# Performance work log

Hardware: AMD Instinct MI355X
Metric: run time of the kernel (lower is better)

## Reference

```python
import jax, jax.numpy as jnp
import numpy as np

K = 2  # DGL TAGConv default number of hops
N_GRAPHS = 64


def _tag_conv(h, src, dst, W, b, norm):
    # TAGConv: concat [h, A_hat h, A_hat^2 h] @ W + b, A_hat = D^-1/2 A D^-1/2
    n = h.shape[0]
    hops = [h]
    cur = h
    for _ in range(K):
        msg = (cur * norm)[src]                      # gather from src, [E, d]
        agg = jnp.zeros_like(cur).at[dst].add(msg)   # scatter-sum to dst
        cur = agg * norm
        hops.append(cur)
    z = jnp.concatenate(hops, axis=-1)               # [N, (K+1)*d]
    return jax.nn.relu(z @ W + b)


def _norm(dst, n):
    deg = jnp.zeros((n,), jnp.float32).at[dst].add(1.0)
    deg = jnp.clip(deg, 1.0, None)
    return (deg ** -0.5)[:, None]                    # [N, 1]


def setup_inputs() -> dict:
    key = jax.random.key(0)
    ks = jax.random.split(key, 8)
    N, E, IN, HID, C = 100000, 3200000, 128, 256, 10
    h = jax.random.normal(ks[0], (N, IN), jnp.float32)
    src = jax.random.randint(ks[1], (E,), 0, N, jnp.int32)
    dst = jax.random.randint(ks[2], (E,), 0, N, jnp.int32)
    graph_ids = jnp.sort(jax.random.randint(ks[3], (N,), 0, N_GRAPHS, jnp.int32))
    s1 = ((K + 1) * IN) ** -0.5
    s2 = ((K + 1) * HID) ** -0.5
    W1 = jax.random.normal(ks[4], ((K + 1) * IN, HID), jnp.float32) * s1
    b1 = jnp.zeros((HID,), jnp.float32)
    W2 = jax.random.normal(ks[5], ((K + 1) * HID, HID), jnp.float32) * s2
    b2 = jnp.zeros((HID,), jnp.float32)
    Wc = jax.random.normal(ks[6], (HID, C), jnp.float32) * (HID ** -0.5)
    bc = jnp.zeros((C,), jnp.float32)
    return {"h": h, "src": src, "dst": dst, "graph_ids": graph_ids,
            "W1": W1, "b1": b1, "W2": W2, "b2": b2, "Wc": Wc, "bc": bc}


def reference(h, src, dst, graph_ids, W1, b1, W2, b2, Wc, bc):
    n = h.shape[0]
    norm = _norm(dst, n)
    x = _tag_conv(h, src, dst, W1, b1, norm)
    x = _tag_conv(x, src, dst, W2, b2, norm)
    pooled = jax.ops.segment_max(x, graph_ids, num_segments=N_GRAPHS)  # [G, HID]
    return pooled @ Wc + bc                                            # [G, C]
```

## Files before the change

kernel.cpp:

```cpp
#include <hip/hip_runtime.h>
#include <hip/hip_bf16.h>


typedef unsigned short u16;
typedef unsigned int u32;
typedef unsigned char u8;

__device__ inline float u2f(u16 u) { return __uint_as_float(((u32)u) << 16); }
__device__ inline u16 f2u(float f) {
    __hip_bfloat16 b = __float2bfloat16(f);
    return *reinterpret_cast<u16*>(&b);
}


constexpr int NPB = 128, NC = 128, NBMAX = 784;

__global__ __launch_bounds__(256) void countA_kernel(
    const int* __restrict__ dst, int* __restrict__ Hmat, int E, int CS, int NB) {
    __shared__ int hist[NBMAX];
    int tid = threadIdx.x;
    for (int b = tid; b < NB; b += 256) hist[b] = 0;
    __syncthreads();
    int base = blockIdx.x * CS;
    int end = base + CS < E ? base + CS : E;
    for (int i = base + tid; i < end; i += 256) {
        int d = __builtin_nontemporal_load(dst + i);
        atomicAdd(&hist[d >> 7], 1);
    }
    __syncthreads();
    for (int b = tid; b < NB; b += 256) Hmat[b * NC + blockIdx.x] = hist[b];
}

__global__ __launch_bounds__(256) void scatterC_kernel(
    const int* __restrict__ src, const int* __restrict__ dst,
    const int* __restrict__ Omat, uint2* __restrict__ Earr,
    int E, int CS, int NB) {
    __shared__ int cur[NBMAX];
    int tid = threadIdx.x;
    int c = blockIdx.x;
    for (int b = tid; b < NB; b += 256) cur[b] = Omat[b * NC + c];
    __syncthreads();
    int base = c * CS;
    int end = base + CS < E ? base + CS : E;
    for (int i = base + tid; i < end; i += 256) {
        int d = __builtin_nontemporal_load(dst + i);
        int s = __builtin_nontemporal_load(src + i);
        int pos = atomicAdd(&cur[d >> 7], 1);
        uint2 e;
        e.x = (u32)s;
        e.y = (u32)(d & (NPB - 1));
        Earr[pos] = e;
    }
}

__global__ __launch_bounds__(256) void fineD_kernel(
    const uint2* __restrict__ Earr, const int* __restrict__ Omat,
    int* __restrict__ colidx, int* __restrict__ rowptr,
    float* __restrict__ normv, int N, int E, int NB) {
    __shared__ int cnt[NPB];
    __shared__ int scn[NPB];
    __shared__ int cur2[NPB];
    int tid = threadIdx.x;
    int b = blockIdx.x;
    int base = Omat[b * NC];
    int end = Omat[(b + 1) * NC];
    if (tid < NPB) cnt[tid] = 0;
    __syncthreads();
    for (int i = base + tid; i < end; i += 256)
        atomicAdd(&cnt[Earr[i].y], 1);
    __syncthreads();
    if (tid < NPB) scn[tid] = cnt[tid];
    __syncthreads();
    for (int off = 1; off < NPB; off <<= 1) {
        int v = (tid < NPB && tid >= off) ? scn[tid - off] : 0;
        __syncthreads();
        if (tid < NPB) scn[tid] += v;
        __syncthreads();
    }
    int node0 = b * NPB;
    if (tid < NPB) {
        int excl = scn[tid] - cnt[tid];
        cur2[tid] = base + excl;
        int node = node0 + tid;
        if (node < N) {
            rowptr[node] = base + excl;
            int d = cnt[tid];
            float fd = d < 1 ? 1.0f : (float)d;
            normv[node] = rsqrtf(fd);
        }
    }
    if (b == 0 && tid == 0) rowptr[N] = E;
    __syncthreads();
    for (int i = base + tid; i < end; i += 256) {
        uint2 e = Earr[i];
        int pos = atomicAdd(&cur2[e.y], 1);
        colidx[pos] = (int)e.x;
    }
}

__global__ void scan1_kernel(const int* __restrict__ in, int* __restrict__ outp,
                             int* __restrict__ bsum, int n) {
    __shared__ int sd[1024];
    int t = threadIdx.x;
    int i = blockIdx.x * 1024 + t;
    int v = (i < n) ? in[i] : 0;
    sd[t] = v;
    __syncthreads();
    for (int off = 1; off < 1024; off <<= 1) {
        int x = (t >= off) ? sd[t - off] : 0;
        __syncthreads();
        sd[t] += x;
        __syncthreads();
    }
    if (i < n) outp[i] = sd[t] - v;
    if (t == 1023) bsum[blockIdx.x] = sd[t];
}

__global__ void scan2_kernel(int* __restrict__ bsum, int nb) {
    __shared__ int sd[1024];
    int t = threadIdx.x;
    int v = (t < nb) ? bsum[t] : 0;
    sd[t] = v;
    __syncthreads();
    for (int off = 1; off < 1024; off <<= 1) {
        int x = (t >= off) ? sd[t - off] : 0;
        __syncthreads();
        sd[t] += x;
        __syncthreads();
    }
    if (t < nb) bsum[t] = sd[t] - v;
}

__global__ void scan3_kernel(int* __restrict__ outp, const int* __restrict__ bsum,
                             int n, int E) {
    int i = blockIdx.x * blockDim.x + threadIdx.x;
    if (i < n) outp[i] += bsum[i >> 10];
    if (i == 0) outp[n] = E;
}


struct alignas(4) U2 { u16 v[2]; };
struct alignas(8) U4 { u16 v[4]; };
struct alignas(16) U8 { u16 v[8]; };


__global__ __launch_bounds__(256) void castquant_f32_128(
    const float* __restrict__ h, u16* __restrict__ cat, int ldcat,
    const float* __restrict__ normv,
    u8* __restrict__ q, float* __restrict__ m, int N) {
    int row = blockIdx.x * 4 + (threadIdx.x >> 6);
    if (row >= N) return;
    int lane = threadIdx.x & 63;
    float2 f = *(const float2*)(h + (size_t)row * 128 + lane * 2);
    U2 o;
    o.v[0] = f2u(f.x);
    o.v[1] = f2u(f.y);
    *(U2*)(cat + (size_t)row * ldcat + lane * 2) = o;
    float mx = fmaxf(fabsf(f.x), fabsf(f.y));
    #pragma unroll
    for (int off = 32; off > 0; off >>= 1)
        mx = fmaxf(mx, __shfl_xor(mx, off, 64));
    float inv = mx > 0.f ? 127.f / mx : 0.f;
    u32 q0 = (u32)((int)rintf(f.x * inv) + 128);
    u32 q1 = (u32)((int)rintf(f.y * inv) + 128);
    *(unsigned short*)(q + (size_t)row * 128 + lane * 2) =
        (unsigned short)(q0 | (q1 << 8));
    if (lane == 0) m[row] = normv[row] * (mx * (1.f / 127.f));
}


__global__ __launch_bounds__(256) void quant_bf16_256(
    const u16* __restrict__ x, const float* __restrict__ normv,
    u8* __restrict__ q, float* __restrict__ m, int N) {
    int row = blockIdx.x * 4 + (threadIdx.x >> 6);
    if (row >= N) return;
    int lane = threadIdx.x & 63;
    U4 v = *(const U4*)(x + (size_t)row * 256 + lane * 4);
    float f[4];
    #pragma unroll
    for (int i = 0; i < 4; ++i) f[i] = u2f(v.v[i]);
    float mx = fmaxf(fmaxf(fabsf(f[0]), fabsf(f[1])),
                     fmaxf(fabsf(f[2]), fabsf(f[3])));
    #pragma unroll
    for (int off = 32; off > 0; off >>= 1)
        mx = fmaxf(mx, __shfl_xor(mx, off, 64));
    float inv = mx > 0.f ? 127.f / mx : 0.f;
    u32 b0 = (u32)((int)rintf(f[0] * inv) + 128);
    u32 b1 = (u32)((int)rintf(f[1] * inv) + 128);
    u32 b2 = (u32)((int)rintf(f[2] * inv) + 128);
    u32 b3 = (u32)((int)rintf(f[3] * inv) + 128);
    *(u32*)(q + (size_t)row * 256 + lane * 4) =
        b0 | (b1 << 8) | (b2 << 16) | (b3 << 24);
    if (lane == 0) m[row] = normv[row] * (mx * (1.f / 127.f));
}


template <int BPL, int QOUT>
__global__ __launch_bounds__(256, 2) void prop_q8_kernel(
    const u8* __restrict__ qin, const float* __restrict__ m,
    u16* __restrict__ out, int ldout,
    const int* __restrict__ rowptr, const int* __restrict__ colidx,
    const float* __restrict__ normv, int N,
    u8* __restrict__ qout, float* __restrict__ mout) {
    constexpr int D = 32 * BPL;
    constexpr int NW = BPL / 4;
    constexpr int UE = 8;
    int node = blockIdx.x * 4 + (threadIdx.x >> 6);
    if (node >= N) return;
    const int lane = threadIdx.x & 63;
    const int half = lane >> 5;
    const int l32 = lane & 31;
    const u32 laneoff = (u32)l32 * BPL;
    int s = rowptr[node], e = rowptr[node + 1];
    float acc[BPL];
    #pragma unroll
    for (int q = 0; q < BPL; ++q) acc[q] = 0.f;
    float msum = 0.f;
    const int nfull = (e - s) >> 4;
    int p = s;
    if (nfull > 0) {
        int c[UE];
        #pragma unroll
        for (int u = 0; u < UE; ++u) c[u] = colidx[s + 2 * u + half];
        for (int g = 0; g < nfull; ++g) {
            u32 w[UE][NW];
            #pragma unroll
            for (int u = 0; u < UE; ++u) {
                u32 off = (u32)c[u] * D + laneoff;
                if (BPL == 8) {
                    uint2 gg = *(const uint2*)(qin + off);
                    w[u][0] = gg.x; w[u][1] = gg.y;
                } else {
                    w[u][0] = *(const u32*)(qin + off);
                }
            }
            float nm[UE];
            #pragma unroll
            for (int u = 0; u < UE; ++u) nm[u] = m[c[u]];
            if (g + 1 < nfull) {
                int pn = s + (g + 1) * 16;
                #pragma unroll
                for (int u = 0; u < UE; ++u) c[u] = colidx[pn + 2 * u + half];
            }
            #pragma unroll
            for (int u = 0; u < UE; ++u) {
                msum += nm[u];
                #pragma unroll
                for (int t = 0; t < NW; ++t) {
                    u32 ww = w[u][t];
                    acc[4 * t + 0] += nm[u] * (float)(ww & 0xffu);
                    acc[4 * t + 1] += nm[u] * (float)((ww >> 8) & 0xffu);
                    acc[4 * t + 2] += nm[u] * (float)((ww >> 16) & 0xffu);
                    acc[4 * t + 3] += nm[u] * (float)(ww >> 24);
                }
            }
        }
        p = s + nfull * 16;
    }
    if (p < e) {
        const int el = e - 1;
        int c[UE];
        #pragma unroll
        for (int u = 0; u < UE; ++u) {
            int idx = p + 2 * u + half;
            c[u] = colidx[idx < e ? idx : el];
        }
        u32 w[UE][NW];
        #pragma unroll
        for (int u = 0; u < UE; ++u) {
            u32 off = (u32)c[u] * D + laneoff;
            if (BPL == 8) {
                uint2 gg = *(const uint2*)(qin + off);
                w[u][0] = gg.x; w[u][1] = gg.y;
            } else {
                w[u][0] = *(const u32*)(qin + off);
            }
        }
        float nm[UE];
        #pragma unroll
        for (int u = 0; u < UE; ++u) {
            int idx = p + 2 * u + half;
            float mm = m[c[u]];
            nm[u] = idx < e ? mm : 0.f;
        }
        #pragma unroll
        for (int u = 0; u < UE; ++u) {
            msum += nm[u];
            #pragma unroll
            for (int t = 0; t < NW; ++t) {
                u32 ww = w[u][t];
                acc[4 * t + 0] += nm[u] * (float)(ww & 0xffu);
                acc[4 * t + 1] += nm[u] * (float)((ww >> 8) & 0xffu);
                acc[4 * t + 2] += nm[u] * (float)((ww >> 16) & 0xffu);
                acc[4 * t + 3] += nm[u] * (float)(ww >> 24);
            }
        }
    }
    #pragma unroll
    for (int q = 0; q < BPL; ++q) acc[q] += __shfl_xor(acc[q], 32, 64);
    msum += __shfl_xor(msum, 32, 64);
    float nn = normv[node];
    #pragma unroll
    for (int q = 0; q < BPL; ++q) acc[q] = nn * (acc[q] - 128.f * msum);
    if (half == 0) {
        if (BPL == 8) {
            U8 o;
            #pragma unroll
            for (int q = 0; q < 8; ++q) o.v[q] = f2u(acc[q]);
            *(U8*)(out + (size_t)node * ldout + l32 * 8) = o;
        } else {
            U4 o;
            #pragma unroll
            for (int q = 0; q < 4; ++q) o.v[q] = f2u(acc[q]);
            *(U4*)(out + (size_t)node * ldout + l32 * 4) = o;
        }
    }
    if (QOUT) {
        float mx = 0.f;
        #pragma unroll
        for (int q = 0; q < BPL; ++q) mx = fmaxf(mx, fabsf(acc[q]));
        #pragma unroll
        for (int off = 16; off > 0; off >>= 1)
            mx = fmaxf(mx, __shfl_xor(mx, off, 64));
        float inv = mx > 0.f ? 127.f / mx : 0.f;
        if (half == 0) {
            u32 b[BPL > 4 ? 8 : 4];
            #pragma unroll
            for (int q = 0; q < BPL; ++q)
                b[q] = (u32)((int)rintf(acc[q] * inv) + 128);
            if (BPL == 8) {
                uint2 g;
                g.x = b[0] | (b[1] << 8) | (b[2] << 16) | (b[3] << 24);
                g.y = b[4] | (b[5] << 8) | (b[6] << 16) | (b[7] << 24);
                *(uint2*)(qout + (size_t)node * D + l32 * 8) = g;
            } else {
                *(u32*)(qout + (size_t)node * D + l32 * 4) =
                    b[0] | (b[1] << 8) | (b[2] << 16) | (b[3] << 24);
            }
            if (lane == 0) mout[node] = nn * (mx * (1.f / 127.f));
        }
    }
}


typedef __attribute__((ext_vector_type(8))) short bf16x8f;
typedef __attribute__((ext_vector_type(4))) float f32x4;

__device__ inline void async16(const void* g, void* l) {
    __builtin_amdgcn_global_load_lds(
        (__attribute__((address_space(1))) void*)(g),
        (__attribute__((address_space(3))) void*)(l), 16, 0, 0);
}

constexpr int GBM = 128, GBN = 128, GBK = 32;

__device__ inline void stage_panel(const u16* __restrict__ P, int ldp, int row0,
                                   int k0, u16* dst, int tid) {
    #pragma unroll
    for (int i = 0; i < 2; ++i) {
        int c = tid + i * 256;
        int row = c >> 2;
        int seg = (c & 3) ^ ((row >> 1) & 3);
        async16(P + (size_t)(row0 + row) * ldp + k0 + seg * 8, dst + c * 8);
    }
}

template <int KK>
__global__ __launch_bounds__(256) void gemm_mfma(
    const u16* __restrict__ A, int lda,
    const u16* __restrict__ Bt,
    const u16* __restrict__ Cadd,
    const float* __restrict__ bias,
    u16* __restrict__ Cout,
    int M, int relu) {
    __shared__ u16 Ab[2][GBM * GBK];
    __shared__ u16 Bb[2][GBN * GBK];
    const int tid = threadIdx.x;
    const int lane = tid & 63;
    const int wave = tid >> 6;
    const int wm = wave >> 1, wn = wave & 1;
    int nwg = gridDim.x;
    int qq = nwg >> 3, rr = nwg & 7;
    int xcd = blockIdx.x & 7, wi = blockIdx.x >> 3;
    int nb = (xcd < rr ? xcd * (qq + 1) : rr * (qq + 1) + (xcd - rr) * qq) + wi;
    const int row0 = (nb >> 1) * GBM;
    const int col0 = (nb & 1) * GBN;
    const int NOUT = 256;

    stage_panel(A, lda, row0, 0, Ab[0], tid);
    stage_panel(Bt, KK, col0, 0, Bb[0], tid);
    __syncthreads();

    f32x4 acc[4][4];
    #pragma unroll
    for (int mi = 0; mi < 4; ++mi)
        #pragma unroll
        for (int ni = 0; ni < 4; ++ni) acc[mi][ni] = (f32x4)0.f;

    constexpr int nk = KK / GBK;
    const int mb = lane & 15;
    const int seg = lane >> 4;
    for (int ks = 0; ks < nk; ++ks) {
        int cur = ks & 1;
        if (ks + 1 < nk) {
            stage_panel(A, lda, row0, (ks + 1) * GBK, Ab[cur ^ 1], tid);
            stage_panel(Bt, KK, col0, (ks + 1) * GBK, Bb[cur ^ 1], tid);
        }
        bf16x8f a[4], b[4];
        #pragma unroll
        for (int mi = 0; mi < 4; ++mi) {
            int r = wm * 64 + mi * 16 + mb;
            int ca = r * 4 + (seg ^ ((r >> 1) & 3));
            a[mi] = *(const bf16x8f*)&Ab[cur][ca * 8];
        }
        #pragma unroll
        for (int ni = 0; ni < 4; ++ni) {
            int n = wn * 64 + ni * 16 + mb;
            int cb = n * 4 + (seg ^ ((n >> 1) & 3));
            b[ni] = *(const bf16x8f*)&Bb[cur][cb * 8];
        }
        #pragma unroll
        for (int mi = 0; mi < 4; ++mi)
            #pragma unroll
            for (int ni = 0; ni < 4; ++ni)
                acc[mi][ni] = __builtin_amdgcn_mfma_f32_16x16x32_bf16(
                    a[mi], b[ni], acc[mi][ni], 0, 0, 0);
        __syncthreads();
    }

    #pragma unroll
    for (int mi = 0; mi < 4; ++mi) {
        #pragma unroll
        for (int r = 0; r < 4; ++r) {
            int row = row0 + wm * 64 + mi * 16 + (lane >> 4) * 4 + r;
            if (row < M) {
                #pragma unroll
                for (int ni = 0; ni < 4; ++ni) {
                    int col = col0 + wn * 64 + ni * 16 + (lane & 15);
                    float v = acc[mi][ni][r];
                    if (Cadd) v += u2f(Cadd[(size_t)row * NOUT + col]);
                    if (bias) v += bias[col];
                    if (relu) v = fmaxf(v, 0.f);
                    Cout[(size_t)row * NOUT + col] = f2u(v);
                }
            }
        }
    }
}

__global__ void transpose_cast(const float* __restrict__ W, u16* __restrict__ Wt,
                               int K, int Nn) {
    int idx = blockIdx.x * blockDim.x + threadIdx.x;
    if (idx < K * Nn) {
        int n = idx / K, k = idx % K;
        Wt[idx] = f2u(W[(size_t)k * Nn + n]);
    }
}


__global__ void pool_kernel(const u16* __restrict__ x, const int* __restrict__ gid,
                            float* __restrict__ pooled, int N, int HID) {
    int t = threadIdx.x;
    int n0 = blockIdx.x * 128;
    int n1 = n0 + 128 < N ? n0 + 128 : N;
    float cur = 0.f;
    int cg = gid[n0];
    for (int n = n0; n < n1; ++n) {
        int g = gid[n];
        if (g != cg) {
            atomicMax((int*)&pooled[(size_t)cg * HID + t], __float_as_int(cur));
            cg = g;
            cur = 0.f;
        }
        float v = u2f(x[(size_t)n * HID + t]);
        cur = cur > v ? cur : v;
    }
    atomicMax((int*)&pooled[(size_t)cg * HID + t], __float_as_int(cur));
}

__global__ void head_kernel(const float* __restrict__ pooled, const float* __restrict__ Wc,
                            const float* __restrict__ bc, float* __restrict__ out,
                            int HID, int C) {
    __shared__ float row[256];
    int g = blockIdx.x;
    int t = threadIdx.x;
    if (t < HID) row[t] = pooled[(size_t)g * HID + t];
    __syncthreads();
    if (t < C) {
        float s = bc[t];
        for (int k = 0; k < HID; ++k) s += row[k] * Wc[(size_t)k * C + t];
        out[(size_t)g * C + t] = s;
    }
}


extern "C" void kernel_launch(void* const* d_in, const int* in_sizes, int n_in,
                              void* d_out, int out_size, void* d_ws, size_t ws_size,
                              hipStream_t stream) {
    const float* h  = (const float*)d_in[0];
    const int* src  = (const int*)d_in[1];
    const int* dst  = (const int*)d_in[2];
    const int* gid  = (const int*)d_in[3];
    const float* W1 = (const float*)d_in[4];
    const float* b1 = (const float*)d_in[5];
    const float* W2 = (const float*)d_in[6];
    const float* b2 = (const float*)d_in[7];
    const float* Wc = (const float*)d_in[8];
    const float* bc = (const float*)d_in[9];
    float* out = (float*)d_out;

    const int N   = in_sizes[3];
    const int E   = in_sizes[1];
    const int IN  = in_sizes[0] / N;
    const int HID = in_sizes[5];
    const int C   = in_sizes[9];
    const int G   = out_size / C;
    const int CAT = 3 * IN;
    const int Mpad = (N + 127) & ~127;
    const int NB = (N + NPB - 1) / NPB;
    const int CS = (E + NC - 1) / NC;

    char* wp = (char*)d_ws;
    auto alloc = [&](size_t bytes) {
        char* p = wp;
        wp += (bytes + 255) & ~(size_t)255;
        return p;
    };
    float* pooled = (float*)alloc((size_t)G * HID * sizeof(float));
    float* normv  = (float*)alloc((size_t)N * sizeof(float));
    float* mv     = (float*)alloc((size_t)N * sizeof(float));
    float* mv2    = (float*)alloc((size_t)N * sizeof(float));
    int* rowptr   = (int*)alloc((size_t)(N + 1) * sizeof(int));
    int* bsum     = (int*)alloc(1024 * sizeof(int));
    int* Omat     = (int*)alloc((size_t)(NB * NC + 1) * sizeof(int));
    int* Hmat     = (int*)alloc((size_t)(NB * NC) * sizeof(int));
    int* colidx   = (int*)alloc((size_t)E * sizeof(int));
    u16* Wt1      = (u16*)alloc((size_t)CAT * HID * sizeof(u16));
    u16* Wt2      = (u16*)alloc((size_t)3 * HID * HID * sizeof(u16));
    u16* CAT1     = (u16*)alloc((size_t)Mpad * CAT * sizeof(u16));
    u16* X1       = (u16*)alloc((size_t)Mpad * HID * sizeof(u16));
    u16* B2       = (u16*)alloc((size_t)Mpad * HID * sizeof(u16));
    u16* B1       = CAT1;
    uint2* Earr   = (uint2*)CAT1;
    u8* Q8L2      = (u8*)(CAT1 + (size_t)Mpad * HID);
    u8* Q8A       = (u8*)B2;
    u8* Q8B       = (u8*)B2 + (size_t)Mpad * 128;

    const int n2 = NB * NC;
    countA_kernel<<<NC, 256, 0, stream>>>(dst, Hmat, E, CS, NB);
    scan1_kernel<<<(n2 + 1023) / 1024, 1024, 0, stream>>>(Hmat, Omat, bsum, n2);
    scan2_kernel<<<1, 1024, 0, stream>>>(bsum, (n2 + 1023) / 1024);
    scan3_kernel<<<(n2 + 255) / 256, 256, 0, stream>>>(Omat, bsum, n2, E);
    scatterC_kernel<<<NC, 256, 0, stream>>>(src, dst, Omat, Earr, E, CS, NB);
    fineD_kernel<<<NB, 256, 0, stream>>>(Earr, Omat, colidx, rowptr, normv, N, E, NB);

    transpose_cast<<<(CAT * HID + 255) / 256, 256, 0, stream>>>(W1, Wt1, CAT, HID);
    for (int s2 = 0; s2 < 3; ++s2)
        transpose_cast<<<(HID * HID + 255) / 256, 256, 0, stream>>>(
            W2 + (size_t)s2 * HID * HID, Wt2 + (size_t)s2 * HID * HID, HID, HID);

    int pb = (N + 3) / 4;
    castquant_f32_128<<<pb, 256, 0, stream>>>(h, CAT1, CAT, normv, Q8A, mv, N);
    prop_q8_kernel<4, 1><<<pb, 256, 0, stream>>>(Q8A, mv, CAT1 + IN, CAT,
                                                 rowptr, colidx, normv, N, Q8B, mv2);
    prop_q8_kernel<4, 0><<<pb, 256, 0, stream>>>(Q8B, mv2, CAT1 + 2 * IN, CAT,
                                                 rowptr, colidx, normv, N,
                                                 nullptr, nullptr);
    int nwg = (Mpad / GBM) * (HID / GBN);
    gemm_mfma<384><<<nwg, 256, 0, stream>>>(CAT1, CAT, Wt1, nullptr, b1, X1, N, 1);

    gemm_mfma<256><<<nwg, 256, 0, stream>>>(X1, HID, Wt2 + (size_t)2 * HID * HID,
                                            nullptr, nullptr, B1, N, 0);
    quant_bf16_256<<<pb, 256, 0, stream>>>(B1, normv, Q8L2, mv, N);
    prop_q8_kernel<8, 0><<<pb, 256, 0, stream>>>(Q8L2, mv, B2, HID,
                                                 rowptr, colidx, normv, N,
                                                 nullptr, nullptr);
    gemm_mfma<256><<<nwg, 256, 0, stream>>>(X1, HID, Wt2 + (size_t)HID * HID,
                                            B2, nullptr, B1, N, 0);
    quant_bf16_256<<<pb, 256, 0, stream>>>(B1, normv, Q8L2, mv, N);
    prop_q8_kernel<8, 0><<<pb, 256, 0, stream>>>(Q8L2, mv, B2, HID,
                                                 rowptr, colidx, normv, N,
                                                 nullptr, nullptr);
    gemm_mfma<256><<<nwg, 256, 0, stream>>>(X1, HID, Wt2, B2, b2, B1, N, 1);

    hipMemsetAsync(pooled, 0, (size_t)G * HID * sizeof(float), stream);
    pool_kernel<<<(N + 127) / 128, HID, 0, stream>>>(B1, gid, pooled, N, HID);
    head_kernel<<<G, HID, 0, stream>>>(pooled, Wc, bc, out, HID, C);
}
```

Baseline: 1.050 ms.

## Stage GEMM K in 128-wide phases instead of double-buffered 32-wide slices

Replaces the double-buffered 32-wide K pipeline with single-buffered 128-wide K phases. Each phase loads the whole panel into LDS with a new XOR swizzle, then runs four MFMA k-steps, which cuts the number of barriers per tile. It also adds a launch_bounds occupancy hint of two blocks per CU. The cost is losing load/compute overlap inside a block, and the 64 KB of LDS per block limits residency.

```diff
diff --git a/kernel.cpp b/kernel.cpp
--- a/kernel.cpp
+++ b/kernel.cpp
@@ -352,29 +352,19 @@
         (__attribute__((address_space(3))) void*)(l), 16, 0, 0);
 }
 
-constexpr int GBM = 128, GBN = 128, GBK = 32;
-
-__device__ inline void stage_panel(const u16* __restrict__ P, int ldp, int row0,
-                                   int k0, u16* dst, int tid) {
-    #pragma unroll
-    for (int i = 0; i < 2; ++i) {
-        int c = tid + i * 256;
-        int row = c >> 2;
-        int seg = (c & 3) ^ ((row >> 1) & 3);
-        async16(P + (size_t)(row0 + row) * ldp + k0 + seg * 8, dst + c * 8);
-    }
-}
+constexpr int GBM = 128, GBN = 128, GBK = 32, KH = 128;
 
 template <int KK>
-__global__ __launch_bounds__(256) void gemm_mfma(
+__global__ __launch_bounds__(256, 2) void gemm_mfma(
     const u16* __restrict__ A, int lda,
     const u16* __restrict__ Bt,
     const u16* __restrict__ Cadd,
     const float* __restrict__ bias,
     u16* __restrict__ Cout,
     int M, int relu) {
-    __shared__ u16 Ab[2][GBM * GBK];
-    __shared__ u16 Bb[2][GBN * GBK];
+    constexpr int NPH = KK / KH;
+    __shared__ u16 Ab[GBM * KH];
+    __shared__ u16 Bb[GBN * KH];
     const int tid = threadIdx.x;
     const int lane = tid & 63;
     const int wave = tid >> 6;
@@ -387,45 +377,57 @@
     const int col0 = (nb & 1) * GBN;
     const int NOUT = 256;
 
-    stage_panel(A, lda, row0, 0, Ab[0], tid);
-    stage_panel(Bt, KK, col0, 0, Bb[0], tid);
-    __syncthreads();
-
     f32x4 acc[4][4];
     #pragma unroll
     for (int mi = 0; mi < 4; ++mi)
         #pragma unroll
         for (int ni = 0; ni < 4; ++ni) acc[mi][ni] = (f32x4)0.f;
 
-    constexpr int nk = KK / GBK;
     const int mb = lane & 15;
-    const int seg = lane >> 4;
-    for (int ks = 0; ks < nk; ++ks) {
-        int cur = ks & 1;
-        if (ks + 1 < nk) {
-            stage_panel(A, lda, row0, (ks + 1) * GBK, Ab[cur ^ 1], tid);
-            stage_panel(Bt, KK, col0, (ks + 1) * GBK, Bb[cur ^ 1], tid);
-        }
-        bf16x8f a[4], b[4];
-        #pragma unroll
-        for (int mi = 0; mi < 4; ++mi) {
-            int r = wm * 64 + mi * 16 + mb;
-            int ca = r * 4 + (seg ^ ((r >> 1) & 3));
-            a[mi] = *(const bf16x8f*)&Ab[cur][ca * 8];
-        }
-        #pragma unroll
-        for (int ni = 0; ni < 4; ++ni) {
-            int n = wn * 64 + ni * 16 + mb;
-            int cb = n * 4 + (seg ^ ((n >> 1) & 3));
-            b[ni] = *(const bf16x8f*)&Bb[cur][cb * 8];
-        }
-        #pragma unroll
-        for (int mi = 0; mi < 4; ++mi)
-            #pragma unroll
-            for (int ni = 0; ni < 4; ++ni)
-                acc[mi][ni] = __builtin_amdgcn_mfma_f32_16x16x32_bf16(
-                    a[mi], b[ni], acc[mi][ni], 0, 0, 0);
-        __syncthreads();
+    const int seg4 = lane >> 4;
+
+    for (int ph = 0; ph < NPH; ++ph) {
+        if (ph) __syncthreads();
+        #pragma unroll
+        for (int i = 0; i < 8; ++i) {
+            int c = tid + i * 256;
+            int row = c >> 4;
+            int sg = (c & 15) ^ (row & 7);
+            async16(A + (size_t)(row0 + row) * lda + ph * KH + sg * 8,
+                    Ab + c * 8);
+        }
+        #pragma unroll
+        for (int i = 0; i < 8; ++i) {
+            int c = tid + i * 256;
+            int row = c >> 4;
+            int sg = (c & 15) ^ (row & 7);
+            async16(Bt + (size_t)(col0 + row) * KK + ph * KH + sg * 8,
+                    Bb + c * 8);
+        }
+        __syncthreads();
+        #pragma unroll
+        for (int ks = 0; ks < KH / GBK; ++ks) {
+            int j = ks * 4 + seg4;
+            bf16x8f a[4], b[4];
+            #pragma unroll
+            for (int mi = 0; mi < 4; ++mi) {
+                int r = wm * 64 + mi * 16 + mb;
+                int ca = r * 16 + (j ^ (r & 7));
+                a[mi] = *(const bf16x8f*)&Ab[ca * 8];
+            }
+            #pragma unroll
+            for (int ni = 0; ni < 4; ++ni) {
+                int n = wn * 64 + ni * 16 + mb;
+                int cb = n * 16 + (j ^ (n & 7));
+                b[ni] = *(const bf16x8f*)&Bb[cb * 8];
+            }
+            #pragma unroll
+            for (int mi = 0; mi < 4; ++mi)
+                #pragma unroll
+                for (int ni = 0; ni < 4; ++ni)
+                    acc[mi][ni] = __builtin_amdgcn_mfma_f32_16x16x32_bf16(
+                        a[mi], b[ni], acc[mi][ni], 0, 0, 0);
+        }
     }
 
     #pragma unroll
```

Measured after the change: 1.012 ms. 1.04x faster.

## Replace LDS-staged GEMM with per-wave register-direct MFMA tiles

Applied to the files above, without the earlier changes.

Swaps the shared-memory double-buffered 128x128 block GEMM for a kernel where each wave independently computes a 128x32 output tile. Each wave loads A and B fragments straight from global memory into registers and feeds them to MFMA, with no LDS staging and no block-level syncs. This removes LDS traffic and barrier overhead and allows more resident blocks per CU. In exchange, the reuse of A across columns now depends on L2/L1 caching instead of shared memory, so each A row panel is fetched by eight separate waves.

```diff
diff --git a/kernel.cpp b/kernel.cpp
--- a/kernel.cpp
+++ b/kernel.cpp
@@ -346,100 +346,73 @@
 typedef __attribute__((ext_vector_type(8))) short bf16x8f;
 typedef __attribute__((ext_vector_type(4))) float f32x4;
 
-__device__ inline void async16(const void* g, void* l) {
-    __builtin_amdgcn_global_load_lds(
-        (__attribute__((address_space(1))) void*)(g),
-        (__attribute__((address_space(3))) void*)(l), 16, 0, 0);
-}
-
-constexpr int GBM = 128, GBN = 128, GBK = 32;
-
-__device__ inline void stage_panel(const u16* __restrict__ P, int ldp, int row0,
-                                   int k0, u16* dst, int tid) {
-    #pragma unroll
-    for (int i = 0; i < 2; ++i) {
-        int c = tid + i * 256;
-        int row = c >> 2;
-        int seg = (c & 3) ^ ((row >> 1) & 3);
-        async16(P + (size_t)(row0 + row) * ldp + k0 + seg * 8, dst + c * 8);
-    }
-}
-
 template <int KK>
-__global__ __launch_bounds__(256) void gemm_mfma(
-    const u16* __restrict__ A, int lda,
+__global__ __launch_bounds__(256, 3) void gemm_wave(
+    const u16* __restrict__ A,
     const u16* __restrict__ Bt,
     const u16* __restrict__ Cadd,
     const float* __restrict__ bias,
     u16* __restrict__ Cout,
-    int M, int relu) {
-    __shared__ u16 Ab[2][GBM * GBK];
-    __shared__ u16 Bb[2][GBN * GBK];
+    int M, int NJOBS, int relu) {
     const int tid = threadIdx.x;
     const int lane = tid & 63;
     const int wave = tid >> 6;
-    const int wm = wave >> 1, wn = wave & 1;
     int nwg = gridDim.x;
     int qq = nwg >> 3, rr = nwg & 7;
     int xcd = blockIdx.x & 7, wi = blockIdx.x >> 3;
-    int nb = (xcd < rr ? xcd * (qq + 1) : rr * (qq + 1) + (xcd - rr) * qq) + wi;
-    const int row0 = (nb >> 1) * GBM;
-    const int col0 = (nb & 1) * GBN;
-    const int NOUT = 256;
-
-    stage_panel(A, lda, row0, 0, Ab[0], tid);
-    stage_panel(Bt, KK, col0, 0, Bb[0], tid);
-    __syncthreads();
-
-    f32x4 acc[4][4];
-    #pragma unroll
-    for (int mi = 0; mi < 4; ++mi)
-        #pragma unroll
-        for (int ni = 0; ni < 4; ++ni) acc[mi][ni] = (f32x4)0.f;
-
-    constexpr int nk = KK / GBK;
+    int slot = (xcd < rr ? xcd * (qq + 1) : rr * (qq + 1) + (xcd - rr) * qq) + wi;
+    int job = slot * 4 + wave;
+    if (job >= NJOBS) return;
+    const int rt = job >> 3;
+    const int cg = job & 7;
+    const int row0 = rt << 7;
+    const int col0 = cg << 5;
     const int mb = lane & 15;
     const int seg = lane >> 4;
-    for (int ks = 0; ks < nk; ++ks) {
-        int cur = ks & 1;
-        if (ks + 1 < nk) {
-            stage_panel(A, lda, row0, (ks + 1) * GBK, Ab[cur ^ 1], tid);
-            stage_panel(Bt, KK, col0, (ks + 1) * GBK, Bb[cur ^ 1], tid);
-        }
-        bf16x8f a[4], b[4];
-        #pragma unroll
-        for (int mi = 0; mi < 4; ++mi) {
-            int r = wm * 64 + mi * 16 + mb;
-            int ca = r * 4 + (seg ^ ((r >> 1) & 3));
-            a[mi] = *(const bf16x8f*)&Ab[cur][ca * 8];
-        }
-        #pragma unroll
-        for (int ni = 0; ni < 4; ++ni) {
-            int n = wn * 64 + ni * 16 + mb;
-            int cb = n * 4 + (seg ^ ((n >> 1) & 3));
-            b[ni] = *(const bf16x8f*)&Bb[cur][cb * 8];
-        }
-        #pragma unroll
-        for (int mi = 0; mi < 4; ++mi)
-            #pragma unroll
-            for (int ni = 0; ni < 4; ++ni)
-                acc[mi][ni] = __builtin_amdgcn_mfma_f32_16x16x32_bf16(
-                    a[mi], b[ni], acc[mi][ni], 0, 0, 0);
-        __syncthreads();
-    }
-
-    #pragma unroll
-    for (int mi = 0; mi < 4; ++mi) {
+    const int NOUT = 256;
+
+    const u16* pA = A + (size_t)(row0 + mb) * KK + seg * 8;
+    const u16* pB = Bt + (size_t)(col0 + mb) * KK + seg * 8;
+
+    f32x4 acc[8][2];
+    #pragma unroll
+    for (int mi = 0; mi < 8; ++mi) {
+        acc[mi][0] = (f32x4)0.f;
+        acc[mi][1] = (f32x4)0.f;
+    }
+
+    #pragma unroll
+    for (int j = 0; j < KK / 32; ++j) {
+        bf16x8f b0 = *(const bf16x8f*)(pB + (size_t)0 * 16 * KK + j * 32);
+        bf16x8f b1 = *(const bf16x8f*)(pB + (size_t)16 * KK + j * 32);
+        bf16x8f a[8];
+        #pragma unroll
+        for (int mi = 0; mi < 8; ++mi)
+            a[mi] = *(const bf16x8f*)(pA + (size_t)mi * 16 * KK + j * 32);
+        #pragma unroll
+        for (int mi = 0; mi < 8; ++mi) {
+            acc[mi][0] = __builtin_amdgcn_mfma_f32_16x16x32_bf16(
+                a[mi], b0, acc[mi][0], 0, 0, 0);
+            acc[mi][1] = __builtin_amdgcn_mfma_f32_16x16x32_bf16(
+                a[mi], b1, acc[mi][1], 0, 0, 0);
+        }
+    }
+
+    float bv[2];
+    bv[0] = bias ? bias[col0 + 0 * 16 + mb] : 0.f;
+    bv[1] = bias ? bias[col0 + 1 * 16 + mb] : 0.f;
+    #pragma unroll
+    for (int mi = 0; mi < 8; ++mi) {
         #pragma unroll
         for (int r = 0; r < 4; ++r) {
-            int row = row0 + wm * 64 + mi * 16 + (lane >> 4) * 4 + r;
+            int row = row0 + mi * 16 + seg * 4 + r;
             if (row < M) {
                 #pragma unroll
-                for (int ni = 0; ni < 4; ++ni) {
-                    int col = col0 + wn * 64 + ni * 16 + (lane & 15);
+                for (int ni = 0; ni < 2; ++ni) {
+                    int col = col0 + ni * 16 + mb;
                     float v = acc[mi][ni][r];
                     if (Cadd) v += u2f(Cadd[(size_t)row * NOUT + col]);
-                    if (bias) v += bias[col];
+                    v += bv[ni];
                     if (relu) v = fmaxf(v, 0.f);
                     Cout[(size_t)row * NOUT + col] = f2u(v);
                 }
@@ -566,22 +539,23 @@
     prop_q8_kernel<4, 0><<<pb, 256, 0, stream>>>(Q8B, mv2, CAT1 + 2 * IN, CAT,
                                                  rowptr, colidx, normv, N,
                                                  nullptr, nullptr);
-    int nwg = (Mpad / GBM) * (HID / GBN);
-    gemm_mfma<384><<<nwg, 256, 0, stream>>>(CAT1, CAT, Wt1, nullptr, b1, X1, N, 1);
-
-    gemm_mfma<256><<<nwg, 256, 0, stream>>>(X1, HID, Wt2 + (size_t)2 * HID * HID,
-                                            nullptr, nullptr, B1, N, 0);
+    const int NJOBS = (Mpad / 128) * 8;
+    const int GW = NJOBS / 4;
+    gemm_wave<384><<<GW, 256, 0, stream>>>(CAT1, Wt1, nullptr, b1, X1, N, NJOBS, 1);
+
+    gemm_wave<256><<<GW, 256, 0, stream>>>(X1, Wt2 + (size_t)2 * HID * HID,
+                                           nullptr, nullptr, B1, N, NJOBS, 0);
     quant_bf16_256<<<pb, 256, 0, stream>>>(B1, normv, Q8L2, mv, N);
     prop_q8_kernel<8, 0><<<pb, 256, 0, stream>>>(Q8L2, mv, B2, HID,
                                                  rowptr, colidx, normv, N,
                                                  nullptr, nullptr);
-    gemm_mfma<256><<<nwg, 256, 0, stream>>>(X1, HID, Wt2 + (size_t)HID * HID,
-                                            B2, nullptr, B1, N, 0);
+    gemm_wave<256><<<GW, 256, 0, stream>>>(X1, HID ? Wt2 + (size_t)HID * HID : Wt2,
+                                           B2, nullptr, B1, N, NJOBS, 0);
     quant_bf16_256<<<pb, 256, 0, stream>>>(B1, normv, Q8L2, mv, N);
     prop_q8_kernel<8, 0><<<pb, 256, 0, stream>>>(Q8L2, mv, B2, HID,
                                                  rowptr, colidx, normv, N,
                                                  nullptr, nullptr);
-    gemm_mfma<256><<<nwg, 256, 0, stream>>>(X1, HID, Wt2, B2, b2, B1, N, 1);
+    gemm_wave<256><<<GW, 256, 0, stream>>>(X1, Wt2, B2, b2, B1, N, NJOBS, 1);
 
     hipMemsetAsync(pooled, 0, (size_t)G * HID * sizeof(float), stream);
     pool_kernel<<<(N + 127) / 128, HID, 0, stream>>>(B1, gid, pooled, N, HID);
```

Result: slower. 1.112 ms (+6.0%).
